# Kernel optimization log

Measured on AMD Instinct MI355X. Metric: run time of the kernel, lower is better.

The kernel has to match this reference:

```python
import jax, jax.numpy as jnp
import numpy as np

D_STATE = 64
HEADDIM = 64
KD = 4

def _layernorm(x, w, b, eps=1e-5):
    m = jnp.mean(x, axis=-1, keepdims=True)
    v = jnp.mean((x - m) ** 2, axis=-1, keepdims=True)
    return (x - m) / jnp.sqrt(v + eps) * w + b

def _adaptive_pool_matrix(n_in, n_out):
    # torch AdaptiveAvgPool2d bin edges: [floor(i*n/o), ceil((i+1)*n/o))
    P = np.zeros((n_out, n_in), np.float32)
    for i in range(n_out):
        s = (i * n_in) // n_out
        e = -((-(i + 1) * n_in) // n_out)
        P[i, s:e] = 1.0 / (e - s)
    return jnp.asarray(P)

def _vss(x, i, vln_w, vln_b, vin_w, vin_b, vconv_w, vconv_b, vxproj_w, vdt_bias, vA_log, vD, von_w, von_b, vout_w, vout_b):
    # VSSBlock (m0_noz): x + SS2D(LayerNorm(x)); x: (Bt, H, W, C) channels-last
    xn = _layernorm(x, vln_w[i], vln_b[i])
    u = xn @ vin_w[i].T + vin_b[i]                      # (Bt,H,W,Din) in_proj (no z branch)
    Bt, H, W, Din = u.shape
    v = jnp.transpose(u, (0, 3, 1, 2))
    v = jax.lax.conv_general_dilated(v, vconv_w[i][:, None], (1, 1), [(1, 1), (1, 1)],
                                     feature_group_count=Din,
                                     dimension_numbers=('NCHW', 'OIHW', 'NCHW'))
    v = v + vconv_b[i][None, :, None, None]
    v = jax.nn.gelu(jnp.transpose(v, (0, 2, 3, 1)))     # depthwise 3x3 + act
    L = H * W
    NH = Din // HEADDIM
    x_row = v.reshape(Bt, L, Din)
    x_col = jnp.transpose(v, (0, 2, 1, 3)).reshape(Bt, L, Din)
    xs = jnp.stack([x_row, x_col, x_row[:, ::-1], x_col[:, ::-1]], 1)  # cross-scan (Bt,KD,L,Din)
    x_dbl = jnp.einsum('bkld,kcd->bklc', xs, vxproj_w[i])              # dt | B | C
    dts = jax.nn.softplus(x_dbl[..., :NH] + vdt_bias[i][None, :, None, :])  # (Bt,KD,L,NH)
    Bm = x_dbl[..., NH:NH + D_STATE]
    Cm = x_dbl[..., NH + D_STATE:]
    A = -jnp.exp(vA_log[i])                             # (KD,NH) scalar-per-head (mamba2)
    xh = xs.reshape(Bt, KD, L, NH, HEADDIM)
    def step(h, t):
        dt_t, x_t, B_t, C_t = t                         # (Bt,KD,NH),(Bt,KD,NH,hd),(Bt,KD,N),(Bt,KD,N)
        dA = jnp.exp(dt_t * A)
        h = h * dA[..., None, None] + (dt_t[..., None] * x_t)[..., None] * B_t[:, :, None, None, :]
        y = jnp.einsum('bkhdn,bkn->bkhd', h, C_t)
        return h, y
    h0 = jnp.zeros((Bt, KD, NH, HEADDIM, D_STATE), x.dtype)
    seq = (jnp.moveaxis(dts, 2, 0), jnp.moveaxis(xh, 2, 0), jnp.moveaxis(Bm, 2, 0), jnp.moveaxis(Cm, 2, 0))
    _, ys = jax.lax.scan(step, h0, seq)                 # (L,Bt,KD,NH,hd)
    ys = jnp.moveaxis(ys, 0, 2) + vD[i][None, :, None, :, None] * xh   # D skip per head
    ys = ys.reshape(Bt, KD, L, Din)
    def uncol(t):
        return jnp.transpose(t.reshape(Bt, W, H, Din), (0, 2, 1, 3)).reshape(Bt, L, Din)
    y = ys[:, 0] + uncol(ys[:, 1]) + ys[:, 2, ::-1] + uncol(ys[:, 3, ::-1])  # cross-merge
    y = _layernorm(y, von_w[i], von_b[i])
    out = y.reshape(Bt, H, W, Din) @ vout_w[i].T + vout_b[i]
    return x + out

def reference(style, mask, content, pos_embed_c, pos_embed_s, newps_w, newps_b,
              vln_w, vln_b, vin_w, vin_b, vconv_w, vconv_b, vxproj_w, vdt_bias, vA_log, vD,
              von_w, von_b, vout_w, vout_b, lin1_w, lin1_b, lin2_w, lin2_b,
              dn1_w, dn1_b, dn2_w, dn2_b, dn3_w, dn3_b, decnorm_w, decnorm_b):
    # mask and the incoming pos_embed_c are unused, matching the torch forward
    B, C, H, W = content.shape
    Ph = _adaptive_pool_matrix(H, 18)
    Pw = _adaptive_pool_matrix(W, 18)
    pooled = jnp.einsum('ih,bchw,jw->bcij', Ph, content, Pw)            # AdaptiveAvgPool2d(18)
    pos_c = jnp.einsum('oc,bcij->boij', newps_w, pooled) + newps_b[None, :, None, None]
    pos_c = jax.image.resize(pos_c, (B, C, style.shape[2], style.shape[3]), method='linear')
    def to_seq(t):  # (B,C,H,W) -> (HW, B, 1, C)
        return jnp.transpose(t.reshape(t.shape[0], t.shape[1], -1), (2, 0, 1))[:, :, None, :]
    s = to_seq(style); c = to_seq(content); ps = to_seq(pos_embed_s); pc = to_seq(pos_c)
    vss = lambda x, i: _vss(x, i, vln_w, vln_b, vin_w, vin_b, vconv_w, vconv_b, vxproj_w,
                            vdt_bias, vA_log, vD, von_w, von_b, vout_w, vout_b)
    s_enc = vss(s, 0)
    c_enc = vss(c, 1)
    q = c_enc + pc
    k = s_enc + ps
    tgt = _layernorm(c_enc + vss(q, 2), dn1_w, dn1_b)
    tgt = tgt + _layernorm(s_enc + vss(k, 3), dn2_w, dn2_b)
    ffn = jax.nn.gelu(tgt @ lin1_w.T + lin1_b) @ lin2_w.T + lin2_b
    tgt = _layernorm(tgt + ffn, dn3_w, dn3_b)
    tgt = _layernorm(tgt, decnorm_w, decnorm_b)
    hs = jnp.transpose(tgt[:, :, 0, :], (1, 2, 0))                      # (B,C,L)
    Hq = int(np.sqrt(hs.shape[-1]))
    return hs.reshape(B, C, -1, Hq)

def setup_inputs():
    key = jax.random.key(0)
    ks = jax.random.split(key, 16)
    D = 512; DIN = 512; NH = DIN // HEADDIM; NB = 4
    f = lambda k, shape, s=0.02: jax.random.normal(k, shape, jnp.float32) * s
    return {
        'style': jax.random.normal(ks[0], (4, 512, 16, 16), jnp.float32),
        'mask': jnp.zeros((4, 256), jnp.bool_),
        'content': jax.random.normal(ks[1], (4, 512, 16, 16), jnp.float32),
        'pos_embed_c': jax.random.normal(ks[2], (4, 512, 16, 16), jnp.float32),
        'pos_embed_s': jax.random.normal(ks[3], (4, 512, 16, 16), jnp.float32),
        'newps_w': f(ks[4], (512, 512)), 'newps_b': jnp.zeros((512,), jnp.float32),
        'vln_w': jnp.ones((NB, D), jnp.float32), 'vln_b': jnp.zeros((NB, D), jnp.float32),
        'vin_w': f(ks[5], (NB, DIN, D)), 'vin_b': jnp.zeros((NB, DIN), jnp.float32),
        'vconv_w': f(ks[6], (NB, DIN, 3, 3), 0.1), 'vconv_b': jnp.zeros((NB, DIN), jnp.float32),
        'vxproj_w': f(ks[7], (NB, KD, NH + 2 * D_STATE, DIN)),
        'vdt_bias': jnp.full((NB, KD, NH), -1.0, jnp.float32),
        'vA_log': f(ks[8], (NB, KD, NH), 0.1),
        'vD': jnp.ones((NB, KD, NH), jnp.float32),
        'von_w': jnp.ones((NB, DIN), jnp.float32), 'von_b': jnp.zeros((NB, DIN), jnp.float32),
        'vout_w': f(ks[9], (NB, D, DIN)), 'vout_b': jnp.zeros((NB, D), jnp.float32),
        'lin1_w': f(ks[10], (2048, D)), 'lin1_b': jnp.zeros((2048,), jnp.float32),
        'lin2_w': f(ks[11], (D, 2048)), 'lin2_b': jnp.zeros((D,), jnp.float32),
        'dn1_w': jnp.ones((D,), jnp.float32), 'dn1_b': jnp.zeros((D,), jnp.float32),
        'dn2_w': jnp.ones((D,), jnp.float32), 'dn2_b': jnp.zeros((D,), jnp.float32),
        'dn3_w': jnp.ones((D,), jnp.float32), 'dn3_b': jnp.zeros((D,), jnp.float32),
        'decnorm_w': jnp.ones((D,), jnp.float32), 'decnorm_b': jnp.zeros((D,), jnp.float32),
    }
```

## Files before the change

kernel.cpp:

```cpp
#include <hip/hip_runtime.h>
#include <hip/hip_bf16.h>
#include <math.h>

#define SEQ   524288
#define MROWS 1024
#define XDBL_P 557056

typedef __hip_bfloat16 bfloat;
typedef __bf16 bfx8 __attribute__((ext_vector_type(8)));
typedef float f32x4 __attribute__((ext_vector_type(4)));

__device__ __forceinline__ float gelu_tanh(float x){
    float x3 = x*x*x;
    float z = 0.7978845608028654f*(x + 0.044715f*x3);
    float az = fabsf(z);
    float e = __expf(-2.f*az);
    float th = copysignf((1.f - e)/(1.f + e), z);
    return 0.5f*x*(1.f + th);
}

__device__ __forceinline__ unsigned short bfbits(float x){
    union { __hip_bfloat16 h; unsigned short u; } cv;
    cv.h = __float2bfloat16(x);
    return cv.u;
}

__device__ __forceinline__ void glds16(const void* g, void* l){
    __builtin_amdgcn_global_load_lds(
        (const __attribute__((address_space(1))) unsigned int*)g,
        (__attribute__((address_space(3))) unsigned int*)l, 16, 0, 0);
}

#define VMWAIT(n) asm volatile("s_waitcnt vmcnt(" #n ")" ::: "memory")

__device__ __forceinline__ void ln_stats(const float* v, float& mean, float& rstd){
    float s = 0.f;
    #pragma unroll
    for (int t = 0; t < 8; ++t) s += v[t];
    #pragma unroll
    for (int off = 32; off > 0; off >>= 1) s += __shfl_xor(s, off, 64);
    mean = s * (1.f/512.f);
    float sq = 0.f;
    #pragma unroll
    for (int t = 0; t < 8; ++t){ float d = v[t] - mean; sq += d*d; }
    #pragma unroll
    for (int off = 32; off > 0; off >>= 1) sq += __shfl_xor(sq, off, 64);
    rstd = rsqrtf(sq * (1.f/512.f) + 1e-5f);
}

struct CvtArgs {
    const float* s[6];
    bfloat* d[6];
    int c4[6];
};
__global__ void cvt_w_kernel(CvtArgs a, int total4){
    int i = blockIdx.x*256 + threadIdx.x;
    if (i >= total4) return;
    int j = 0, base = 0;
    while (j < 5 && i >= a.c4[j]) { base = a.c4[j]; ++j; }
    int k = i - base;
    float4 v = ((const float4*)a.s[j])[k];
    union { bfloat h[4]; ushort4 u; } o;
    o.h[0] = __float2bfloat16(v.x); o.h[1] = __float2bfloat16(v.y);
    o.h[2] = __float2bfloat16(v.z); o.h[3] = __float2bfloat16(v.w);
    *(ushort4*)(a.d[j] + (size_t)k*4) = o.u;
}

__global__ void to_seq3_kernel(const float* __restrict__ s, const float* __restrict__ c,
                               const float* __restrict__ p,
                               float* __restrict__ os, float* __restrict__ oc,
                               float* __restrict__ op){
    __shared__ float t[32][33];
    int blk = blockIdx.x;
    int lt = blk & 7;  blk >>= 3;
    int ct = blk & 15; blk >>= 4;
    int b  = blk & 3;  blk >>= 2;
    const float* in = blk==0 ? s : (blk==1 ? c : p);
    float* o = blk==0 ? os : (blk==1 ? oc : op);
    int c0 = ct*32, l0 = lt*32;
    int lx = threadIdx.x & 31, g = threadIdx.x >> 5;
    #pragma unroll
    for (int q = 0; q < 4; ++q){
        int cy = g + q*8;
        t[cy][lx] = in[(size_t)(b*512 + c0+cy)*256 + l0 + lx];
    }
    __syncthreads();
    #pragma unroll
    for (int q = 0; q < 4; ++q){
        int ly = g + q*8;
        o[((size_t)(l0+ly)*4 + b)*512 + c0 + lx] = t[lx][ly];
    }
}

__global__ void from_seq_kernel(const float* __restrict__ in, float* __restrict__ out){
    int idx = blockIdx.x*256 + threadIdx.x;
    int l = idx & 255;
    int c = (idx >> 8) & 511;
    int b = idx >> 17;
    out[idx] = in[(size_t)(l*4 + b)*512 + c];
}

__global__ void pool_kernel(const float* __restrict__ content, bfloat* __restrict__ pooledT){
    int bij = blockIdx.x;
    int b = bij / 324;
    int ij = bij % 324;
    int i = ij / 18, j = ij % 18;
    int s0 = (i*16)/18,  e0 = ((i+1)*16 + 17)/18;
    int s1 = (j*16)/18,  e1 = ((j+1)*16 + 17)/18;
    float inv = 1.0f / (float)((e0-s0)*(e1-s1));
    for (int c = threadIdx.x; c < 512; c += 256){
        float acc = 0.f;
        for (int h = s0; h < e0; ++h)
            for (int w = s1; w < e1; ++w)
                acc += content[((b*512 + c)*16 + h)*16 + w];
        pooledT[(size_t)(b*324 + ij)*512 + c] = __float2bfloat16(acc * inv);
    }
}

__device__ __forceinline__ int resize_taps(int o, float* w, int* j0_out){
    const float inv_scale = 18.0f/16.0f;
    float sf = (o + 0.5f)*inv_scale - 0.5f;
    int j0 = (int)ceilf(sf - inv_scale);
    int j1 = (int)floorf(sf + inv_scale);
    if (j0 < 0) j0 = 0;
    if (j1 > 17) j1 = 17;
    int n = j1 - j0 + 1;
    float sum = 0.f;
    for (int t = 0; t < n; ++t){
        float d = fabsf(sf - (float)(j0 + t)) * (16.0f/18.0f);
        float v = fmaxf(0.f, 1.f - d);
        w[t] = v; sum += v;
    }
    float r = 1.f / sum;
    for (int t = 0; t < n; ++t) w[t] *= r;
    *j0_out = j0;
    return n;
}

__global__ void resize_kernel(const float* __restrict__ pc18T, float* __restrict__ pc_seq){
    int bid = blockIdx.x;
    int b = bid >> 8;
    int yx = bid & 255;
    int y = yx >> 4, x = yx & 15;
    float wy[3], wx[3];
    int jy0, jx0;
    int ny = resize_taps(y, wy, &jy0);
    int nx = resize_taps(x, wx, &jx0);
    for (int c = threadIdx.x; c < 512; c += 256){
        float acc = 0.f;
        for (int ty = 0; ty < ny; ++ty)
            for (int tx = 0; tx < nx; ++tx)
                acc += wy[ty]*wx[tx] *
                       pc18T[(size_t)(b*324 + (jy0+ty)*18 + (jx0+tx))*512 + c];
        pc_seq[(size_t)((y*16 + x)*4 + b)*512 + c] = acc;
    }
}

__global__ __launch_bounds__(256) void ln_vss_pair_kernel(
    const float* __restrict__ x0, const float* __restrict__ x20,
    const float* __restrict__ x1, const float* __restrict__ x21,
    const float* __restrict__ wall, const float* __restrict__ ball,
    int ibase, bfloat* __restrict__ outb)
{
    int row = blockIdx.x*4 + (threadIdx.x >> 6);
    int lane = threadIdx.x & 63;
    int p = row >> 10, r2 = row & 1023;
    const float* in0 = (p ? x1 : x0) + (size_t)r2*512;
    const float* in1 = p ? x21 : x20;
    const float* w = wall + (ibase+p)*512;
    const float* b = ball + (ibase+p)*512;
    int base = lane*8;
    float v[8];
    #pragma unroll
    for (int t = 0; t < 8; ++t){
        v[t] = in0[base + t];
        if (in1) v[t] += in1[(size_t)r2*512 + base + t];
    }
    float mean, rstd;
    ln_stats(v, mean, rstd);
    bfloat* o = outb + (size_t)p*SEQ + (size_t)r2*512 + base;
    union { ushort u[8]; uint4 q; } pk;
    #pragma unroll
    for (int t = 0; t < 8; ++t)
        pk.u[t] = bfbits((v[t] - mean)*rstd*w[base + t] + b[base + t]);
    *(uint4*)o = pk.q;
}

__global__ __launch_bounds__(256) void dn_pair_kernel(
    const float* __restrict__ a0, const float* __restrict__ a1,
    const float* __restrict__ w1, const float* __restrict__ b1,
    const float* __restrict__ c0, const float* __restrict__ c1,
    const float* __restrict__ w2, const float* __restrict__ b2,
    float* __restrict__ outf, bfloat* __restrict__ outb)
{
    int row = blockIdx.x*4 + (threadIdx.x >> 6);
    int lane = threadIdx.x & 63;
    int base = lane*8;
    size_t ro = (size_t)row*512 + base;
    float va[8], vc[8];
    #pragma unroll
    for (int t = 0; t < 8; ++t){ va[t] = a0[ro+t] + a1[ro+t]; vc[t] = c0[ro+t] + c1[ro+t]; }
    float m1, r1, m2, r2;
    ln_stats(va, m1, r1);
    ln_stats(vc, m2, r2);
    union { ushort u[8]; uint4 q; } pk;
    #pragma unroll
    for (int t = 0; t < 8; ++t){
        float o = (va[t]-m1)*r1*w1[base+t] + b1[base+t]
                + (vc[t]-m2)*r2*w2[base+t] + b2[base+t];
        outf[ro + t] = o;
        pk.u[t] = bfbits(o);
    }
    *(uint4*)(outb + ro) = pk.q;
}

__global__ __launch_bounds__(256) void ln2_kernel(
    const float* __restrict__ in0, const float* __restrict__ in1,
    const float* __restrict__ w1, const float* __restrict__ b1,
    const float* __restrict__ w2, const float* __restrict__ b2,
    float* __restrict__ out)
{
    int row = blockIdx.x*4 + (threadIdx.x >> 6);
    int lane = threadIdx.x & 63;
    int base = lane*8;
    size_t ro = (size_t)row*512 + base;
    float v[8];
    #pragma unroll
    for (int t = 0; t < 8; ++t) v[t] = in0[ro+t] + in1[ro+t];
    float mean, rstd;
    ln_stats(v, mean, rstd);
    #pragma unroll
    for (int t = 0; t < 8; ++t) v[t] = (v[t]-mean)*rstd*w1[base+t] + b1[base+t];
    ln_stats(v, mean, rstd);
    #pragma unroll
    for (int t = 0; t < 8; ++t)
        out[ro + t] = (v[t]-mean)*rstd*w2[base+t] + b2[base+t];
}

struct GJob {
    const bfloat* A; const bfloat* W;
    const float* bias; const float* res1; const float* res2;
    float* Cf; bfloat* Cb;
    const float* cw; const float* cb;
    float* v; float* vr; bfloat* vb; bfloat* vrb;
};

__global__ __launch_bounds__(256) void gemm3_kernel(
    GJob J0, GJob J1, GJob J2, GJob J3,
    int M, int N, int K, int nbn, int epi)
{
    __shared__ __align__(16) char lds[65536];
    const int z = blockIdx.z;
    GJob j = (z==0) ? J0 : (z==1) ? J1 : (z==2) ? J2 : J3;

    int nwg = gridDim.x;
    int orig = blockIdx.x;
    int q = nwg >> 3, r = nwg & 7;
    int xcd = orig & 7, off = orig >> 3;
    int wgid = (xcd < r ? xcd*(q+1) : r*(q+1) + (xcd-r)*q) + off;
    int bm = (wgid / nbn) * 64;
    int bn = (wgid % nbn) * 64;

    const int tid = threadIdx.x;
    const int wv = tid >> 6, ln = tid & 63;

    const int r0 = tid >> 3;
    const int cs = (tid & 7) ^ (r0 & 7);
    int ar0 = bm + r0;       if (ar0 > M-1) ar0 = M-1;
    int ar1 = bm + r0 + 32;  if (ar1 > M-1) ar1 = M-1;
    int br0 = bn + r0;       if (br0 > N-1) br0 = N-1;
    int br1 = bn + r0 + 32;  if (br1 > N-1) br1 = N-1;
    const bfloat* a0p = j.A + (size_t)ar0*K + cs*8;
    const bfloat* a1p = j.A + (size_t)ar1*K + cs*8;
    const bfloat* b0p = j.W + (size_t)br0*K + cs*8;
    const bfloat* b1p = j.W + (size_t)br1*K + cs*8;

    auto STAGE = [&](int bb, int k0){
        char* base = lds + bb*16384 + wv*1024;
        glds16(a0p + k0, base);
        glds16(a1p + k0, base + 4096);
        glds16(b0p + k0, base + 8192);
        glds16(b1p + k0, base + 12288);
    };

    const int wr = wv >> 1, wc = wv & 1;
    const int fr = ln & 15, fc = ln >> 4;
    f32x4 acc[2][2] = {};

    auto COMP = [&](int bb){
        char* bA = lds + bb*16384;
        char* bB = bA + 8192;
        int ra0 = wr*32 + fr, ra1 = ra0 + 16;
        int rb0 = wc*32 + fr, rb1 = rb0 + 16;
        #pragma unroll
        for (int kk = 0; kk < 2; ++kk){
            int ch = kk*4 + fc;
            bfx8 a0 = *(const bfx8*)(bA + ra0*128 + ((ch ^ (ra0&7))<<4));
            bfx8 a1 = *(const bfx8*)(bA + ra1*128 + ((ch ^ (ra1&7))<<4));
            bfx8 b0 = *(const bfx8*)(bB + rb0*128 + ((ch ^ (rb0&7))<<4));
            bfx8 b1 = *(const bfx8*)(bB + rb1*128 + ((ch ^ (rb1&7))<<4));
            acc[0][0] = __builtin_amdgcn_mfma_f32_16x16x32_bf16(a0,b0,acc[0][0],0,0,0);
            acc[0][1] = __builtin_amdgcn_mfma_f32_16x16x32_bf16(a0,b1,acc[0][1],0,0,0);
            acc[1][0] = __builtin_amdgcn_mfma_f32_16x16x32_bf16(a1,b0,acc[1][0],0,0,0);
            acc[1][1] = __builtin_amdgcn_mfma_f32_16x16x32_bf16(a1,b1,acc[1][1],0,0,0);
        }
    };

    const int nt = K >> 6;
    for (int s = 0; s < 3 && s < nt; ++s) STAGE(s, s << 6);
    for (int t = 0; t < nt; ++t){
        int rem = nt - 1 - t;
        if (rem >= 2)      VMWAIT(8);
        else if (rem == 1) VMWAIT(4);
        else               VMWAIT(0);
        __builtin_amdgcn_sched_barrier(0);
        __builtin_amdgcn_s_barrier();
        if (t + 3 < nt) STAGE((t+3) & 3, (t+3) << 6);
        COMP(t & 3);
    }

    const int er = (ln >> 4) * 4;
    const int ec = ln & 15;

    if (epi == 2){
        __syncthreads();
        float* ut = (float*)lds;
        #pragma unroll
        for (int i = 0; i < 2; ++i)
        #pragma unroll
        for (int jj = 0; jj < 2; ++jj)
        #pragma unroll
        for (int rr = 0; rr < 4; ++rr){
            int ml = wr*32 + i*16 + er + rr;
            int nl = wc*32 + jj*16 + ec;
            ut[ml*65 + nl] = acc[i][jj][rr] + j.bias[bn + nl];
        }
        __syncthreads();
        int rrow = tid >> 2, c0 = (tid & 3) * 16;
        int bt4 = rrow & ~3, lv = rrow & 3;
        int m = bm + rrow;
        int mrev = bm + bt4 + 3 - lv;
        float g[16];
        #pragma unroll
        for (int c = 0; c < 16; ++c){
            int n = bn + c0 + c;
            float a = j.cb[n];
            #pragma unroll
            for (int kh = 0; kh < 3; ++kh){
                int hh = lv + kh - 1;
                if (hh >= 0 && hh < 4)
                    a += ut[(bt4 + hh)*65 + c0 + c] * j.cw[(n*3 + kh)*3 + 1];
            }
            g[c] = gelu_tanh(a);
        }
        #pragma unroll
        for (int c = 0; c < 16; c += 4){
            float4 f = make_float4(g[c], g[c+1], g[c+2], g[c+3]);
            *(float4*)(j.v + (size_t)m*512 + bn + c0 + c) = f;
        }
        union { ushort u[8]; uint4 qv; } pk;
        #pragma unroll
        for (int h = 0; h < 2; ++h){
            #pragma unroll
            for (int t = 0; t < 8; ++t) pk.u[t] = bfbits(g[h*8 + t]);
            *(uint4*)(j.vb  + (size_t)m   *512 + bn + c0 + h*8) = pk.qv;
            *(uint4*)(j.vrb + (size_t)mrev*512 + bn + c0 + h*8) = pk.qv;
        }
        return;
    }

    #pragma unroll
    for (int i = 0; i < 2; ++i)
    #pragma unroll
    for (int jj = 0; jj < 2; ++jj)
    #pragma unroll
    for (int rr = 0; rr < 4; ++rr){
        int m = bm + wr*32 + i*16 + er + rr;
        int n = bn + wc*32 + jj*16 + ec;
        if (m >= M || n >= N) continue;
        float v = acc[i][jj][rr];
        if (j.bias) v += j.bias[n];
        if (epi == 1) v = gelu_tanh(v);
        if (j.res1) v += j.res1[(size_t)m*N + n];
        if (j.res2) v += j.res2[(size_t)m*N + n];
        if (epi == 3){
            int k2 = n >= 136;
            int cc = n - (k2 ? 136 : 0);
            j.Cf[((size_t)(k2*1024 + m))*136 + cc] = v;
        } else {
            if (j.Cf) j.Cf[(size_t)m*N + n] = v;
            if (j.Cb) j.Cb[(size_t)m*N + n] = __float2bfloat16(v);
        }
    }
}

__global__ __launch_bounds__(256) void scan_fused_kernel(
    const float* __restrict__ xdbl,
    const float* __restrict__ v,
    const float* __restrict__ dt_bias,
    const float* __restrict__ A_log,
    const float* __restrict__ Dp,
    const float* __restrict__ von_w, const float* __restrict__ von_b,
    int ibase, bfloat* __restrict__ outb)
{
    __shared__ float yb[4][4][512];
    int blk = blockIdx.x;
    int p = blk >> 8, bt = blk & 255;
    int k = threadIdx.x >> 6, lane = threadIdx.x & 63;

    const float* xd = xdbl + (size_t)p*XDBL_P + (size_t)(k*1024 + bt*4)*136;

    float bb[4], cc[4];
    #pragma unroll
    for (int l = 0; l < 4; ++l){
        bb[l] = xd[l*136 + 8 + lane];
        cc[l] = xd[l*136 + 72 + lane];
    }

    int sl = (lane & 31) >> 3, snh = lane & 7;
    float Aval = -expf(A_log[p*32 + k*8 + snh]);
    float draw = xd[sl*136 + snh] + dt_bias[p*32 + k*8 + snh];
    float dtv = fmaxf(draw, 0.f) + log1pf(expf(-fabsf(draw)));
    float dAv = expf(dtv * Aval);

    float s[16];
    #pragma unroll
    for (int l = 0; l < 4; ++l)
    #pragma unroll
    for (int jj = 0; jj < 4; ++jj)
        s[l*4+jj] = cc[l]*bb[jj];
    #pragma unroll
    for (int off = 32; off > 0; off >>= 1)
        #pragma unroll
        for (int i = 0; i < 16; ++i)
            s[i] += __shfl_xor(s[i], off, 64);

    float x[4][8];
    #pragma unroll
    for (int lp = 0; lp < 4; ++lp){
        int row = bt*4 + ((k < 2) ? lp : 3 - lp);
        const float* xr = v + (size_t)p*SEQ + (size_t)row*512 + lane;
        #pragma unroll
        for (int nh = 0; nh < 8; ++nh) x[lp][nh] = xr[nh*64];
    }

    #pragma unroll
    for (int nh = 0; nh < 8; ++nh){
        float dtl[4], dal[4];
        #pragma unroll
        for (int l = 0; l < 4; ++l){
            dtl[l] = __shfl(dtv, l*8 + nh, 64);
            dal[l] = __shfl(dAv, l*8 + nh, 64);
        }
        float Dv = Dp[p*32 + k*8 + nh];
        float coef[4] = {0.f, 0.f, 0.f, 0.f};
        #pragma unroll
        for (int l = 0; l < 4; ++l){
            #pragma unroll
            for (int jj = 0; jj < 4; ++jj) coef[jj] *= dal[l];
            coef[l] = dtl[l];
            float y = Dv * x[l][nh];
            #pragma unroll
            for (int jj = 0; jj <= l; ++jj) y += coef[jj]*s[l*4+jj]*x[jj][nh];
            yb[k][l][nh*64 + lane] = y;
        }
    }
    __syncthreads();

    int l = k, rl = 3 - k;
    int base = lane*8;
    float vv[8];
    #pragma unroll
    for (int t = 0; t < 8; ++t)
        vv[t] = yb[0][l][base+t] + yb[1][l][base+t]
              + yb[2][rl][base+t] + yb[3][rl][base+t];
    float mean, rstd;
    ln_stats(vv, mean, rstd);
    const float* w = von_w + (ibase+p)*512;
    const float* bv = von_b + (ibase+p)*512;
    union { ushort u[8]; uint4 qv; } pk;
    #pragma unroll
    for (int t = 0; t < 8; ++t)
        pk.u[t] = bfbits((vv[t]-mean)*rstd*w[base+t] + bv[base+t]);
    *(uint4*)(outb + (size_t)p*SEQ + (size_t)(bt*4 + l)*512 + base) = pk.qv;
}

extern "C" void kernel_launch(void* const* d_in, const int* in_sizes, int n_in,
                              void* d_out, int out_size, void* d_ws, size_t ws_size,
                              hipStream_t stream)
{
    const float* style   = (const float*)d_in[0];
    const float* content = (const float*)d_in[2];
    const float* pos_s   = (const float*)d_in[4];
    const float* newps_w = (const float*)d_in[5];
    const float* newps_b = (const float*)d_in[6];
    const float* vln_w   = (const float*)d_in[7];
    const float* vln_b   = (const float*)d_in[8];
    const float* vin_b   = (const float*)d_in[10];
    const float* vconv_w = (const float*)d_in[11];
    const float* vconv_b = (const float*)d_in[12];
    const float* vdt_bias= (const float*)d_in[14];
    const float* vA_log  = (const float*)d_in[15];
    const float* vD      = (const float*)d_in[16];
    const float* von_w   = (const float*)d_in[17];
    const float* von_b   = (const float*)d_in[18];
    const float* vout_b  = (const float*)d_in[20];
    const float* lin1_b  = (const float*)d_in[22];
    const float* lin2_b  = (const float*)d_in[24];
    const float* dn1_w   = (const float*)d_in[25];
    const float* dn1_b   = (const float*)d_in[26];
    const float* dn2_w   = (const float*)d_in[27];
    const float* dn2_b   = (const float*)d_in[28];
    const float* dn3_w   = (const float*)d_in[29];
    const float* dn3_b   = (const float*)d_in[30];
    const float* decn_w  = (const float*)d_in[31];
    const float* decn_b  = (const float*)d_in[32];

    float* out = (float*)d_out;
    float* ws  = (float*)d_ws;

    float* s_seq  = ws + (size_t) 0*SEQ;
    float* c_seq  = ws + (size_t) 1*SEQ;
    float* ps_seq = ws + (size_t) 2*SEQ;
    float* pc_seq = ws + (size_t) 3*SEQ;
    float* s_enc  = ws + (size_t) 4*SEQ;
    float* c_enc  = ws + (size_t) 5*SEQ;
    float* t1     = ws + (size_t) 6*SEQ;
    float* t2     = ws + (size_t) 7*SEQ;
    float* tgt    = ws + (size_t) 8*SEQ;
    float* ffnout = ws + (size_t) 9*SEQ;
    float* vbuf   = ws + (size_t)10*SEQ;
    float* xdbl   = ws + (size_t)12*SEQ;
    float* pc18T  = ws + (size_t)15*SEQ;
    float* tgt3   = vbuf;

    bfloat* wb = (bfloat*)(ws + (size_t)17*SEQ);
    bfloat* wb_vin    = wb;
    bfloat* wb_xproj  = wb + 1048576;
    bfloat* wb_vout   = wb + 2162688;
    bfloat* wb_lin1   = wb + 3211264;
    bfloat* wb_lin2   = wb + 4259840;
    bfloat* wb_newps  = wb + 5308416;
    bfloat* xn_bf     = wb + 5570560;
    bfloat* vbuf_bf   = xn_bf   + (size_t)2*SEQ;
    bfloat* vrev_bf   = vbuf_bf + (size_t)2*SEQ;
    bfloat* tgt_bf    = vrev_bf + (size_t)2*SEQ;
    bfloat* ffn_bf    = tgt_bf  + (size_t)SEQ;
    bfloat* pooled_bf = ffn_bf;

    auto launch_gemm = [&](GJob* jobs, int nz, int M, int N, int K, int epi){
        int nbm = (M + 63)/64, nbn = (N + 63)/64;
        dim3 g(nbm*nbn, 1, nz);
        gemm3_kernel<<<g, 256, 0, stream>>>(jobs[0], jobs[nz>1?1:0],
                                            jobs[nz>2?2:0], jobs[nz>3?3:0],
                                            M, N, K, nbn, epi);
    };

    GJob Z = {};

    auto vss_pair = [&](const float* xa, const float* x2a,
                        const float* xb, const float* x2b,
                        int ibase, float* oa, float* ob){
        ln_vss_pair_kernel<<<512, 256, 0, stream>>>(xa, x2a, xb, x2b,
                                                    vln_w, vln_b, ibase, xn_bf);
        GJob jv[2];
        for (int p = 0; p < 2; ++p){
            int i = ibase + p;
            jv[p] = Z;
            jv[p].A = xn_bf + (size_t)p*SEQ;
            jv[p].W = wb_vin + (size_t)i*262144;
            jv[p].bias = vin_b + i*512;
            jv[p].cw = vconv_w + (size_t)i*4608;
            jv[p].cb = vconv_b + i*512;
            jv[p].v   = vbuf + (size_t)p*SEQ;
            jv[p].vb  = vbuf_bf + (size_t)p*SEQ;
            jv[p].vrb = vrev_bf + (size_t)p*SEQ;
        }
        launch_gemm(jv, 2, MROWS, 512, 512, 2);

        GJob jx[4];
        for (int zz = 0; zz < 4; ++zz){
            int p = zz >> 1, rev = zz & 1, i = ibase + p;
            jx[zz] = Z;
            jx[zz].A = (rev ? vrev_bf : vbuf_bf) + (size_t)p*SEQ;
            jx[zz].W = wb_xproj + (size_t)i*278528 + (size_t)rev*272*512;
            jx[zz].Cf = xdbl + (size_t)p*XDBL_P + (size_t)rev*278528;
        }
        launch_gemm(jx, 4, MROWS, 272, 512, 3);

        scan_fused_kernel<<<512, 256, 0, stream>>>(xdbl, vbuf,
                                                   vdt_bias + ibase*32,
                                                   vA_log + ibase*32,
                                                   vD + ibase*32,
                                                   von_w, von_b, ibase, xn_bf);

        GJob jo[2];
        const float* r1[2] = {xa, xb};
        const float* r2[2] = {x2a, x2b};
        float* oo[2] = {oa, ob};
        for (int p = 0; p < 2; ++p){
            int i = ibase + p;
            jo[p] = Z;
            jo[p].A = xn_bf + (size_t)p*SEQ;
            jo[p].W = wb_vout + (size_t)i*262144;
            jo[p].bias = vout_b + i*512;
            jo[p].res1 = r1[p];
            jo[p].res2 = r2[p];
            jo[p].Cf = oo[p];
        }
        launch_gemm(jo, 2, MROWS, 512, 512, 0);
    };

    CvtArgs ca;
    ca.s[0]=(const float*)d_in[9];  ca.d[0]=wb_vin;
    ca.s[1]=(const float*)d_in[13]; ca.d[1]=wb_xproj;
    ca.s[2]=(const float*)d_in[19]; ca.d[2]=wb_vout;
    ca.s[3]=(const float*)d_in[21]; ca.d[3]=wb_lin1;
    ca.s[4]=(const float*)d_in[23]; ca.d[4]=wb_lin2;
    ca.s[5]=newps_w;                ca.d[5]=wb_newps;
    ca.c4[0]=262144; ca.c4[1]=540672; ca.c4[2]=802816;
    ca.c4[3]=1064960; ca.c4[4]=1327104; ca.c4[5]=1392640;
    cvt_w_kernel<<<(1392640+255)/256, 256, 0, stream>>>(ca, 1392640);

    to_seq3_kernel<<<1536, 256, 0, stream>>>(style, content, pos_s,
                                             s_seq, c_seq, ps_seq);
    pool_kernel<<<1296, 256, 0, stream>>>(content, pooled_bf);
    GJob jn = Z;
    jn.A = pooled_bf; jn.W = wb_newps; jn.bias = newps_b; jn.Cf = pc18T;
    launch_gemm(&jn, 1, 1296, 512, 512, 0);
    resize_kernel<<<1024, 256, 0, stream>>>(pc18T, pc_seq);

    vss_pair(s_seq, nullptr, c_seq, nullptr, 0, s_enc, c_enc);

    vss_pair(c_enc, pc_seq, s_enc, ps_seq, 2, t1, t2);
    dn_pair_kernel<<<256, 256, 0, stream>>>(c_enc, t1, dn1_w, dn1_b,
                                            s_enc, t2, dn2_w, dn2_b,
                                            tgt, tgt_bf);

    GJob jf = Z;
    jf.A = tgt_bf; jf.W = wb_lin1; jf.bias = lin1_b; jf.Cb = ffn_bf;
    launch_gemm(&jf, 1, MROWS, 2048, 512, 1);
    GJob jg = Z;
    jg.A = ffn_bf; jg.W = wb_lin2; jg.bias = lin2_b; jg.Cf = ffnout;
    launch_gemm(&jg, 1, MROWS, 512, 2048, 0);
    ln2_kernel<<<256, 256, 0, stream>>>(tgt, ffnout, dn3_w, dn3_b,
                                        decn_w, decn_b, tgt3);
    from_seq_kernel<<<SEQ/256, 256, 0, stream>>>(tgt3, out);
}
```

Baseline: 171.9 us.

## Merge prep kernels, fuse output transpose, drop reversed and fp32 conv buffers

Three setup kernels (weight convert, transpose to sequence, pooling) become one prep kernel selected by block ranges, which removes two launches. The final layernorm now writes straight into the output layout, so the separate from_seq transpose is gone. The conv epilogue no longer writes an fp32 copy or a reversed bf16 copy. The xproj GEMM instead reads rows in reversed order through a row-index remap, and the scan reads bf16 activations. This cuts memory traffic and launch count, but the scan now reads the activations as bf16 rather than fp32, which lowers precision.

```diff
diff --git a/kernel.cpp b/kernel.cpp
--- a/kernel.cpp
+++ b/kernel.cpp
@@ -53,67 +53,62 @@
     bfloat* d[6];
     int c4[6];
 };
-__global__ void cvt_w_kernel(CvtArgs a, int total4){
-    int i = blockIdx.x*256 + threadIdx.x;
-    if (i >= total4) return;
-    int j = 0, base = 0;
-    while (j < 5 && i >= a.c4[j]) { base = a.c4[j]; ++j; }
-    int k = i - base;
-    float4 v = ((const float4*)a.s[j])[k];
-    union { bfloat h[4]; ushort4 u; } o;
-    o.h[0] = __float2bfloat16(v.x); o.h[1] = __float2bfloat16(v.y);
-    o.h[2] = __float2bfloat16(v.z); o.h[3] = __float2bfloat16(v.w);
-    *(ushort4*)(a.d[j] + (size_t)k*4) = o.u;
-}
-
-__global__ void to_seq3_kernel(const float* __restrict__ s, const float* __restrict__ c,
-                               const float* __restrict__ p,
-                               float* __restrict__ os, float* __restrict__ oc,
-                               float* __restrict__ op){
-    __shared__ float t[32][33];
+__global__ void prep_kernel(CvtArgs a,
+                            const float* __restrict__ style,
+                            const float* __restrict__ content,
+                            const float* __restrict__ pos_s,
+                            float* __restrict__ s_seq, float* __restrict__ c_seq,
+                            float* __restrict__ ps_seq,
+                            bfloat* __restrict__ pooledT)
+{
+    __shared__ float tsh[32][33];
     int blk = blockIdx.x;
-    int lt = blk & 7;  blk >>= 3;
-    int ct = blk & 15; blk >>= 4;
-    int b  = blk & 3;  blk >>= 2;
-    const float* in = blk==0 ? s : (blk==1 ? c : p);
-    float* o = blk==0 ? os : (blk==1 ? oc : op);
-    int c0 = ct*32, l0 = lt*32;
-    int lx = threadIdx.x & 31, g = threadIdx.x >> 5;
-    #pragma unroll
-    for (int q = 0; q < 4; ++q){
-        int cy = g + q*8;
-        t[cy][lx] = in[(size_t)(b*512 + c0+cy)*256 + l0 + lx];
-    }
-    __syncthreads();
-    #pragma unroll
-    for (int q = 0; q < 4; ++q){
-        int ly = g + q*8;
-        o[((size_t)(l0+ly)*4 + b)*512 + c0 + lx] = t[lx][ly];
-    }
-}
-
-__global__ void from_seq_kernel(const float* __restrict__ in, float* __restrict__ out){
-    int idx = blockIdx.x*256 + threadIdx.x;
-    int l = idx & 255;
-    int c = (idx >> 8) & 511;
-    int b = idx >> 17;
-    out[idx] = in[(size_t)(l*4 + b)*512 + c];
-}
-
-__global__ void pool_kernel(const float* __restrict__ content, bfloat* __restrict__ pooledT){
-    int bij = blockIdx.x;
-    int b = bij / 324;
-    int ij = bij % 324;
-    int i = ij / 18, j = ij % 18;
-    int s0 = (i*16)/18,  e0 = ((i+1)*16 + 17)/18;
-    int s1 = (j*16)/18,  e1 = ((j+1)*16 + 17)/18;
-    float inv = 1.0f / (float)((e0-s0)*(e1-s1));
-    for (int c = threadIdx.x; c < 512; c += 256){
-        float acc = 0.f;
-        for (int h = s0; h < e0; ++h)
-            for (int w = s1; w < e1; ++w)
-                acc += content[((b*512 + c)*16 + h)*16 + w];
-        pooledT[(size_t)(b*324 + ij)*512 + c] = __float2bfloat16(acc * inv);
+    int tid = threadIdx.x;
+    if (blk < 5440){
+        int i = blk*256 + tid;
+        int j = 0, base = 0;
+        while (j < 5 && i >= a.c4[j]) { base = a.c4[j]; ++j; }
+        int k = i - base;
+        float4 v = ((const float4*)a.s[j])[k];
+        union { bfloat h[4]; ushort4 u; } o;
+        o.h[0] = __float2bfloat16(v.x); o.h[1] = __float2bfloat16(v.y);
+        o.h[2] = __float2bfloat16(v.z); o.h[3] = __float2bfloat16(v.w);
+        *(ushort4*)(a.d[j] + (size_t)k*4) = o.u;
+    } else if (blk < 6976){
+        int b2 = blk - 5440;
+        int lt = b2 & 7;  b2 >>= 3;
+        int ct = b2 & 15; b2 >>= 4;
+        int b  = b2 & 3;  b2 >>= 2;
+        const float* in = b2==0 ? style : (b2==1 ? content : pos_s);
+        float* o = b2==0 ? s_seq : (b2==1 ? c_seq : ps_seq);
+        int c0 = ct*32, l0 = lt*32;
+        int lx = tid & 31, g = tid >> 5;
+        #pragma unroll
+        for (int qq = 0; qq < 4; ++qq){
+            int cy = g + qq*8;
+            tsh[cy][lx] = in[(size_t)(b*512 + c0+cy)*256 + l0 + lx];
+        }
+        __syncthreads();
+        #pragma unroll
+        for (int qq = 0; qq < 4; ++qq){
+            int ly = g + qq*8;
+            o[((size_t)(l0+ly)*4 + b)*512 + c0 + lx] = tsh[lx][ly];
+        }
+    } else {
+        int bij = blk - 6976;
+        int b = bij / 324;
+        int ij = bij % 324;
+        int i = ij / 18, jc = ij % 18;
+        int s0 = (i*16)/18,  e0 = ((i+1)*16 + 17)/18;
+        int s1 = (jc*16)/18, e1 = ((jc+1)*16 + 17)/18;
+        float inv = 1.0f / (float)((e0-s0)*(e1-s1));
+        for (int c = tid; c < 512; c += 256){
+            float acc = 0.f;
+            for (int h = s0; h < e0; ++h)
+                for (int w = s1; w < e1; ++w)
+                    acc += content[((b*512 + c)*16 + h)*16 + w];
+            pooledT[(size_t)(b*324 + ij)*512 + c] = __float2bfloat16(acc * inv);
+        }
     }
 }
 
@@ -214,7 +209,7 @@
     *(uint4*)(outb + ro) = pk.q;
 }
 
-__global__ __launch_bounds__(256) void ln2_kernel(
+__global__ __launch_bounds__(256) void ln2_out_kernel(
     const float* __restrict__ in0, const float* __restrict__ in1,
     const float* __restrict__ w1, const float* __restrict__ b1,
     const float* __restrict__ w2, const float* __restrict__ b2,
@@ -232,9 +227,12 @@
     #pragma unroll
     for (int t = 0; t < 8; ++t) v[t] = (v[t]-mean)*rstd*w1[base+t] + b1[base+t];
     ln_stats(v, mean, rstd);
-    #pragma unroll
-    for (int t = 0; t < 8; ++t)
-        out[ro + t] = (v[t]-mean)*rstd*w2[base+t] + b2[base+t];
+    int l = row >> 2, b = row & 3;
+    #pragma unroll
+    for (int t = 0; t < 8; ++t){
+        float o = (v[t]-mean)*rstd*w2[base+t] + b2[base+t];
+        out[(size_t)(b*512 + base + t)*256 + l] = o;
+    }
 }
 
 struct GJob {
@@ -242,7 +240,8 @@
     const float* bias; const float* res1; const float* res2;
     float* Cf; bfloat* Cb;
     const float* cw; const float* cb;
-    float* v; float* vr; bfloat* vb; bfloat* vrb;
+    bfloat* vb;
+    int arev;
 };
 
 __global__ __launch_bounds__(256) void gemm3_kernel(
@@ -268,6 +267,7 @@
     const int cs = (tid & 7) ^ (r0 & 7);
     int ar0 = bm + r0;       if (ar0 > M-1) ar0 = M-1;
     int ar1 = bm + r0 + 32;  if (ar1 > M-1) ar1 = M-1;
+    if (j.arev){ ar0 = (ar0 & ~3) | (3 - (ar0 & 3)); ar1 = (ar1 & ~3) | (3 - (ar1 & 3)); }
     int br0 = bn + r0;       if (br0 > N-1) br0 = N-1;
     int br1 = bn + r0 + 32;  if (br1 > N-1) br1 = N-1;
     const bfloat* a0p = j.A + (size_t)ar0*K + cs*8;
@@ -339,7 +339,6 @@
         int rrow = tid >> 2, c0 = (tid & 3) * 16;
         int bt4 = rrow & ~3, lv = rrow & 3;
         int m = bm + rrow;
-        int mrev = bm + bt4 + 3 - lv;
         float g[16];
         #pragma unroll
         for (int c = 0; c < 16; ++c){
@@ -353,18 +352,12 @@
             }
             g[c] = gelu_tanh(a);
         }
-        #pragma unroll
-        for (int c = 0; c < 16; c += 4){
-            float4 f = make_float4(g[c], g[c+1], g[c+2], g[c+3]);
-            *(float4*)(j.v + (size_t)m*512 + bn + c0 + c) = f;
-        }
         union { ushort u[8]; uint4 qv; } pk;
         #pragma unroll
         for (int h = 0; h < 2; ++h){
             #pragma unroll
             for (int t = 0; t < 8; ++t) pk.u[t] = bfbits(g[h*8 + t]);
-            *(uint4*)(j.vb  + (size_t)m   *512 + bn + c0 + h*8) = pk.qv;
-            *(uint4*)(j.vrb + (size_t)mrev*512 + bn + c0 + h*8) = pk.qv;
+            *(uint4*)(j.vb + (size_t)m*512 + bn + c0 + h*8) = pk.qv;
         }
         return;
     }
@@ -396,7 +389,7 @@
 
 __global__ __launch_bounds__(256) void scan_fused_kernel(
     const float* __restrict__ xdbl,
-    const float* __restrict__ v,
+    const bfloat* __restrict__ vb,
     const float* __restrict__ dt_bias,
     const float* __restrict__ A_log,
     const float* __restrict__ Dp,
@@ -439,9 +432,9 @@
     #pragma unroll
     for (int lp = 0; lp < 4; ++lp){
         int row = bt*4 + ((k < 2) ? lp : 3 - lp);
-        const float* xr = v + (size_t)p*SEQ + (size_t)row*512 + lane;
-        #pragma unroll
-        for (int nh = 0; nh < 8; ++nh) x[lp][nh] = xr[nh*64];
+        const bfloat* xr = vb + (size_t)p*SEQ + (size_t)row*512 + lane;
+        #pragma unroll
+        for (int nh = 0; nh < 8; ++nh) x[lp][nh] = __bfloat162float(xr[nh*64]);
     }
 
     #pragma unroll
@@ -529,12 +522,10 @@
     float* t2     = ws + (size_t) 7*SEQ;
     float* tgt    = ws + (size_t) 8*SEQ;
     float* ffnout = ws + (size_t) 9*SEQ;
-    float* vbuf   = ws + (size_t)10*SEQ;
-    float* xdbl   = ws + (size_t)12*SEQ;
-    float* pc18T  = ws + (size_t)15*SEQ;
-    float* tgt3   = vbuf;
-
-    bfloat* wb = (bfloat*)(ws + (size_t)17*SEQ);
+    float* xdbl   = ws + (size_t)10*SEQ;
+    float* pc18T  = ws + (size_t)13*SEQ;
+
+    bfloat* wb = (bfloat*)(ws + (size_t)15*SEQ);
     bfloat* wb_vin    = wb;
     bfloat* wb_xproj  = wb + 1048576;
     bfloat* wb_vout   = wb + 2162688;
@@ -543,8 +534,7 @@
     bfloat* wb_newps  = wb + 5308416;
     bfloat* xn_bf     = wb + 5570560;
     bfloat* vbuf_bf   = xn_bf   + (size_t)2*SEQ;
-    bfloat* vrev_bf   = vbuf_bf + (size_t)2*SEQ;
-    bfloat* tgt_bf    = vrev_bf + (size_t)2*SEQ;
+    bfloat* tgt_bf    = vbuf_bf + (size_t)2*SEQ;
     bfloat* ffn_bf    = tgt_bf  + (size_t)SEQ;
     bfloat* pooled_bf = ffn_bf;
 
@@ -572,9 +562,7 @@
             jv[p].bias = vin_b + i*512;
             jv[p].cw = vconv_w + (size_t)i*4608;
             jv[p].cb = vconv_b + i*512;
-            jv[p].v   = vbuf + (size_t)p*SEQ;
-            jv[p].vb  = vbuf_bf + (size_t)p*SEQ;
-            jv[p].vrb = vrev_bf + (size_t)p*SEQ;
+            jv[p].vb = vbuf_bf + (size_t)p*SEQ;
         }
         launch_gemm(jv, 2, MROWS, 512, 512, 2);
 
@@ -582,13 +570,14 @@
         for (int zz = 0; zz < 4; ++zz){
             int p = zz >> 1, rev = zz & 1, i = ibase + p;
             jx[zz] = Z;
-            jx[zz].A = (rev ? vrev_bf : vbuf_bf) + (size_t)p*SEQ;
+            jx[zz].A = vbuf_bf + (size_t)p*SEQ;
+            jx[zz].arev = rev;
             jx[zz].W = wb_xproj + (size_t)i*278528 + (size_t)rev*272*512;
             jx[zz].Cf = xdbl + (size_t)p*XDBL_P + (size_t)rev*278528;
         }
         launch_gemm(jx, 4, MROWS, 272, 512, 3);
 
-        scan_fused_kernel<<<512, 256, 0, stream>>>(xdbl, vbuf,
+        scan_fused_kernel<<<512, 256, 0, stream>>>(xdbl, vbuf_bf,
                                                    vdt_bias + ibase*32,
                                                    vA_log + ibase*32,
                                                    vD + ibase*32,
@@ -620,11 +609,9 @@
     ca.s[5]=newps_w;                ca.d[5]=wb_newps;
     ca.c4[0]=262144; ca.c4[1]=540672; ca.c4[2]=802816;
     ca.c4[3]=1064960; ca.c4[4]=1327104; ca.c4[5]=1392640;
-    cvt_w_kernel<<<(1392640+255)/256, 256, 0, stream>>>(ca, 1392640);
-
-    to_seq3_kernel<<<1536, 256, 0, stream>>>(style, content, pos_s,
-                                             s_seq, c_seq, ps_seq);
-    pool_kernel<<<1296, 256, 0, stream>>>(content, pooled_bf);
+    prep_kernel<<<8272, 256, 0, stream>>>(ca, style, content, pos_s,
+                                          s_seq, c_seq, ps_seq, pooled_bf);
+
     GJob jn = Z;
     jn.A = pooled_bf; jn.W = wb_newps; jn.bias = newps_b; jn.Cf = pc18T;
     launch_gemm(&jn, 1, 1296, 512, 512, 0);
@@ -643,7 +630,6 @@
     GJob jg = Z;
     jg.A = ffn_bf; jg.W = wb_lin2; jg.bias = lin2_b; jg.Cf = ffnout;
     launch_gemm(&jg, 1, MROWS, 512, 2048, 0);
-    ln2_kernel<<<256, 256, 0, stream>>>(tgt, ffnout, dn3_w, dn3_b,
-                                        decn_w, decn_b, tgt3);
-    from_seq_kernel<<<SEQ/256, 256, 0, stream>>>(tgt3, out);
-}
+    ln2_out_kernel<<<256, 256, 0, stream>>>(tgt, ffnout, dn3_w, dn3_b,
+                                            decn_w, decn_b, out);
+}
```

Result: faster. 166.1 us, median of 2 (-3.4%).
